# Performance work log

Measured on AMD Instinct MI355X. Metric: run time of the kernel, lower is better.

The kernel has to match this reference:

```python
import jax, jax.numpy as jnp
import numpy as np

EPS = 1e-7  # keras backend.epsilon()


def _conv_relu(x, w, b):
    # ConvNormRelu with BatchNorm folded into conv bias at inference
    y = jax.lax.conv_general_dilated(x, w, (1, 1), 'SAME',
                                     dimension_numbers=('NHWC', 'HWIO', 'NHWC'))
    return jax.nn.relu(y + b)


def _mlp(x, mw0, mb0, mw1, mb1, mw2, mb2):
    h = jax.nn.relu(x @ mw0 + mb0)
    h = jax.nn.relu(h @ mw1 + mb1)
    return h @ mw2 + mb2


def setup_inputs() -> dict:
    key = jax.random.key(0)
    ks = jax.random.split(key, 20)
    B, HQ = 2, 384
    feats2 = jax.random.normal(ks[0], (B, 192, 192, 64), jnp.float32)
    feats4 = jax.random.normal(ks[1], (B, 96, 96, 96), jnp.float32)
    feats32 = jax.random.normal(ks[2], (B, 24, 24, 160), jnp.float32)
    coords = jax.random.uniform(ks[3], (B, HQ, HQ, 2), jnp.float32, -1.0, 1.0)
    cells = jnp.full((B, HQ, HQ, 2), 2.0 / HQ, jnp.float32)
    s = 0.05
    params = dict(
        w2=jax.random.normal(ks[4], (1, 1, 64, 32)) * s, b2=jnp.zeros((32,)),
        w4=jax.random.normal(ks[5], (1, 1, 96, 32)) * s, b4=jnp.zeros((32,)),
        w32=jax.random.normal(ks[6], (1, 1, 160, 32)) * s, b32=jnp.zeros((32,)),
        wf=jax.random.normal(ks[7], (3, 3, 96, 96)) * s, bf=jnp.zeros((96,)),
        mw0=jax.random.normal(ks[8], (102, 64)) * s, mb0=jnp.zeros((64,)),
        mw1=jax.random.normal(ks[9], (64, 64)) * s, mb1=jnp.zeros((64,)),
        mw2=jax.random.normal(ks[10], (64, 1)) * s, mb2=jnp.zeros((1,)),
    )
    return dict(feats2=feats2, feats4=feats4, feats32=feats32,
                coords=coords, cells=cells, **params)


def reference(feats2, feats4, feats32, coords, cells,
              w2, b2, w4, b4, w32, b32, wf, bf,
              mw0, mb0, mw1, mb1, mw2, mb2):
    a2 = _conv_relu(feats2, w2, b2)
    a4 = _conv_relu(feats4, w4, b4)
    a32 = _conv_relu(feats32, w32, b32)
    B, H, W, _ = a2.shape
    # resize_by_sample: bilinear upsample to feats2 grid (half-pixel centers)
    a4 = jax.image.resize(a4, (B, H, W, a4.shape[-1]), method='bilinear')
    a32 = jax.image.resize(a32, (B, H, W, a32.shape[-1]), method='bilinear')
    aspp = _conv_relu(jnp.concatenate([a2, a4, a32], axis=-1), wf, bf)

    size = jnp.array([H, W], jnp.float32)
    rxry = 1.0 / size
    rel_cells = cells * size
    bi = jnp.arange(B)[:, None, None]  # batch gather index

    preds, areas = [], []
    for vy in (-1.0, 1.0):  # itertools.product([-1,1],[-1,1]) order
        for vx in (-1.0, 1.0):
            vv = jnp.array([vy, vx], jnp.float32)
            c = jnp.clip(coords + vv * rxry + EPS, -1.0 + EPS, 1.0 - EPS)
            # original reverses (y,x)->(x,y) for GridSample; index directly instead
            # nearest, align_corners=False: i = round((c+1)*N/2 - 0.5)
            iy = jnp.clip(jnp.round((c[..., 0] + 1.0) * H / 2.0 - 0.5).astype(jnp.int32), 0, H - 1)
            ix = jnp.clip(jnp.round((c[..., 1] + 1.0) * W / 2.0 - 0.5).astype(jnp.int32), 0, W - 1)
            feat_samp = aspp[bi, iy, ix]  # [B,HQ,WQ,96] irregular gather
            # nearest-sampling make_coord == analytic pixel centers of (iy,ix)
            coord_samp = jnp.stack(
                [((iy.astype(jnp.float32) + 0.5) / H) * 2.0 - 1.0,
                 ((ix.astype(jnp.float32) + 0.5) / W) * 2.0 - 1.0], axis=-1)
            rel = (coords - coord_samp) * size
            pred = _mlp(jnp.concatenate([feat_samp, rel, coords, rel_cells], axis=-1),
                        mw0, mb0, mw1, mb1, mw2, mb2)
            preds.append(pred)
            area = jnp.abs(jnp.prod(rel, axis=-1, keepdims=True)) + EPS
            areas.insert(0, area)  # pair each pred with opposite corner's area

    num = preds[0] * areas[0] + preds[1] * areas[1] + preds[2] * areas[2] + preds[3] * areas[3]
    den = areas[0] + areas[1] + areas[2] + areas[3]
    return num / den
```

## Files before the change

### kernel.cpp

```cpp
#include <hip/hip_runtime.h>
#include <math.h>


#define HQ 384
#define HA 192
#define NQ (2 * HQ * HQ)
#define NBS (NQ / 1024)
#define NBKT 288
#define NFLAT (NBKT * NBS)

typedef _Float16 half8  __attribute__((ext_vector_type(8)));
typedef _Float16 half4v __attribute__((ext_vector_type(4)));
typedef float    float4v __attribute__((ext_vector_type(4)));
typedef float    float16v __attribute__((ext_vector_type(16)));

__device__ __forceinline__ int bucket_id(int q, float cy, float cx) {
    const float LO = -1.0f + 1e-7f, HI = 1.0f - 1e-7f;
    const float RXY = 1.0f / (float)HA;
    float c0 = fminf(fmaxf((cy - RXY) + 1e-7f, LO), HI);
    float c1 = fminf(fmaxf((cx - RXY) + 1e-7f, LO), HI);
    int iy = (int)rintf(((c0 + 1.f) * (float)HA) * 0.5f - 0.5f);
    int ix = (int)rintf(((c1 + 1.f) * (float)HA) * 0.5f - 0.5f);
    iy = min(max(iy, 0), HA - 1);
    ix = min(max(ix, 0), HA - 1);
    int b = q / (HQ * HQ);
    return b * 144 + (iy >> 4) * 12 + (ix >> 4);
}

__launch_bounds__(1024)
__global__ void fused_front(const float* __restrict__ coords,
                            int* __restrict__ cntT,
                            unsigned short* __restrict__ lrank,
                            const float* __restrict__ mw0,
                            const float* __restrict__ mb0f,
                            const float* __restrict__ mw1,
                            const float* __restrict__ mb1f,
                            const float* __restrict__ wf,
                            _Float16* __restrict__ fragTab,
                            _Float16* __restrict__ fragTabW,
                            const float* __restrict__ feats4,
                            const float* __restrict__ w4,
                            const float* __restrict__ b4,
                            const float* __restrict__ feats32,
                            const float* __restrict__ w32,
                            const float* __restrict__ b32,
                            float* __restrict__ a4s,
                            float* __restrict__ a32s,
                            const float* __restrict__ feats2,
                            const float* __restrict__ w2,
                            const float* __restrict__ b2,
                            _Float16* __restrict__ xcatH) {
    const int blk = blockIdx.x;
    const int tid = threadIdx.x;

    if (blk < 288) {
        __shared__ int lh[NBKT];
        if (tid < NBKT) lh[tid] = 0;
        __syncthreads();
        const int q = blk * 1024 + tid;
        float cy = coords[(size_t)q * 2 + 0];
        float cx = coords[(size_t)q * 2 + 1];
        int r = atomicAdd(&lh[bucket_id(q, cy, cx)], 1);
        lrank[q] = (unsigned short)r;
        __syncthreads();
        if (tid < NBKT) cntT[tid * NBS + blk] = lh[tid];
    } else if (blk < 300) {
        int t = (blk - 288) * 1024 + tid;
        if (t < 1536) {
            int f = t >> 6, L = t & 63;
            int h = L >> 5;
            _Float16 vals[8];
            if (f < 14) {
                int ks = f >> 1, nt = f & 1;
                int col = nt * 32 + (L & 31);
#pragma unroll
                for (int j = 0; j < 8; ++j) {
                    int kk = ks * 16 + h * 8 + j;
                    float v = (kk < 102) ? mw0[kk * 64 + col]
                            : ((kk == 102) ? mb0f[col] : 0.f);
                    vals[j] = (_Float16)v;
                }
            } else {
                int g = f - 14;
                int ks = g >> 1, nt = g & 1;
                int col = nt * 32 + (L & 31);
#pragma unroll
                for (int j = 0; j < 8; ++j) {
                    int kp = ks * 16 + h * 8 + j;
                    float v;
                    if (ks < 4) {
                        int n = (kp & 0x33) | ((kp & 8) >> 1) | ((kp & 4) << 1);
                        v = mw1[n * 64 + col];
                    } else {
                        v = (kp == 64) ? mb1f[col] : 0.f;
                    }
                    vals[j] = (_Float16)v;
                }
            }
#pragma unroll
            for (int j = 0; j < 8; ++j) fragTab[t * 8 + j] = vals[j];
        } else {
            int tw = t - 1536;
            if (tw < 27 * 6 * 64) {
                int s   = tw / 384;
                int rem = tw - s * 384;
                int nt  = rem >> 6;
                int L   = rem & 63;
                int n_  = L & 15, qd = L >> 4;
                int tap = s / 3, kc = s - tap * 3;
#pragma unroll
                for (int j = 0; j < 8; ++j) {
                    int kch = kc * 32 + qd * 8 + j;
                    fragTabW[tw * 8 + j] =
                        (_Float16)wf[(tap * 96 + kch) * 96 + nt * 16 + n_];
                }
            }
        }
    } else if (blk < 444) {
        int t = (blk - 300) * 1024 + tid;
        int p = t >> 3, cg = t & 7;
        const float4v* xr = (const float4v*)(feats4 + (size_t)p * 96);
        float4v acc = *(const float4v*)(b4 + cg * 4);
#pragma unroll
        for (int i4 = 0; i4 < 24; ++i4) {
            float4v xv = xr[i4];
            const float* wr = w4 + (i4 * 4) * 32 + cg * 4;
#pragma unroll
            for (int j = 0; j < 4; ++j) {
                float4v wv = *(const float4v*)(wr + j * 32);
                acc[0] = fmaf(xv[j], wv[0], acc[0]);
                acc[1] = fmaf(xv[j], wv[1], acc[1]);
                acc[2] = fmaf(xv[j], wv[2], acc[2]);
                acc[3] = fmaf(xv[j], wv[3], acc[3]);
            }
        }
        float4v o = {fmaxf(acc[0], 0.f), fmaxf(acc[1], 0.f),
                     fmaxf(acc[2], 0.f), fmaxf(acc[3], 0.f)};
        *(float4v*)(a4s + (size_t)p * 32 + cg * 4) = o;
    } else if (blk < 453) {
        int t = (blk - 444) * 1024 + tid;
        if (t >= 1152 * 8) return;
        int p = t >> 3, cg = t & 7;
        const float4v* xr = (const float4v*)(feats32 + (size_t)p * 160);
        float4v acc = *(const float4v*)(b32 + cg * 4);
#pragma unroll
        for (int i4 = 0; i4 < 40; ++i4) {
            float4v xv = xr[i4];
            const float* wr = w32 + (i4 * 4) * 32 + cg * 4;
#pragma unroll
            for (int j = 0; j < 4; ++j) {
                float4v wv = *(const float4v*)(wr + j * 32);
                acc[0] = fmaf(xv[j], wv[0], acc[0]);
                acc[1] = fmaf(xv[j], wv[1], acc[1]);
                acc[2] = fmaf(xv[j], wv[2], acc[2]);
                acc[3] = fmaf(xv[j], wv[3], acc[3]);
            }
        }
        float4v o = {fmaxf(acc[0], 0.f), fmaxf(acc[1], 0.f),
                     fmaxf(acc[2], 0.f), fmaxf(acc[3], 0.f)};
        *(float4v*)(a32s + (size_t)p * 32 + cg * 4) = o;
    } else {
        int t = (blk - 453) * 1024 + tid;
        int p = t >> 3, cg = t & 7;
        const float4v* xr = (const float4v*)(feats2 + (size_t)p * 64);
        float4v acc = *(const float4v*)(b2 + cg * 4);
#pragma unroll
        for (int i4 = 0; i4 < 16; ++i4) {
            float4v xv = xr[i4];
            const float* wr = w2 + (i4 * 4) * 32 + cg * 4;
#pragma unroll
            for (int j = 0; j < 4; ++j) {
                float4v wv = *(const float4v*)(wr + j * 32);
                acc[0] = fmaf(xv[j], wv[0], acc[0]);
                acc[1] = fmaf(xv[j], wv[1], acc[1]);
                acc[2] = fmaf(xv[j], wv[2], acc[2]);
                acc[3] = fmaf(xv[j], wv[3], acc[3]);
            }
        }
        half4v h;
        h[0] = (_Float16)fmaxf(acc[0], 0.f);
        h[1] = (_Float16)fmaxf(acc[1], 0.f);
        h[2] = (_Float16)fmaxf(acc[2], 0.f);
        h[3] = (_Float16)fmaxf(acc[3], 0.f);
        *(half4v*)(xcatH + (size_t)p * 96 + cg * 4) = h;
    }
}

__launch_bounds__(1024)
__global__ void fused_mid(const int* __restrict__ cntT,
                          int* __restrict__ scanEx,
                          int* __restrict__ chunkTot,
                          const float* __restrict__ a4s,
                          const float* __restrict__ a32s,
                          _Float16* __restrict__ xcatH) {
    const int blk = blockIdx.x;
    const int t = threadIdx.x;

    if (blk < 81) {
        __shared__ int s[1024];
        const int gi = blk * 1024 + t;
        int v = cntT[gi];
        s[t] = v;
        __syncthreads();
        for (int off = 1; off < 1024; off <<= 1) {
            int x = (t >= off) ? s[t - off] : 0;
            __syncthreads();
            s[t] += x;
            __syncthreads();
        }
        scanEx[gi] = s[t] - v;
        if (t == 1023) chunkTot[blk] = s[t];
        return;
    }

    const int z = (blk < 81 + 576) ? 1 : 2;
    int tt = ((z == 1) ? (blk - 81) : (blk - 657)) * 1024 + t;
    int p = tt >> 3, cg = tt & 7;

    const float* src = (z == 1) ? a4s : a32s;
    const int   S    = (z == 1) ? 96 : 24;
    const float inv  = (z == 1) ? 0.5f : 0.125f;
    const int   coff = (z == 1) ? 32 : 64;

    int x = p % HA;
    int r = p / HA;
    int y = r % HA;
    int b = r / HA;

    float u = ((float)y + 0.5f) * inv - 0.5f;
    float v = ((float)x + 0.5f) * inv - 0.5f;
    float fu = floorf(u), fv = floorf(v);
    float wu = u - fu, wv = v - fv;
    int y0 = (int)fu, x0 = (int)fv;
    int y1 = min(y0 + 1, S - 1);
    int x1 = min(x0 + 1, S - 1);
    y0 = max(y0, 0);
    x0 = max(x0, 0);

    const float* sb = src + (size_t)b * S * S * 32 + cg * 4;
    float4v v00 = *(const float4v*)(sb + (y0 * S + x0) * 32);
    float4v v01 = *(const float4v*)(sb + (y0 * S + x1) * 32);
    float4v v10 = *(const float4v*)(sb + (y1 * S + x0) * 32);
    float4v v11 = *(const float4v*)(sb + (y1 * S + x1) * 32);
    half4v h;
#pragma unroll
    for (int j = 0; j < 4; ++j) {
        float t0 = v00[j] * (1.f - wu) + v10[j] * wu;
        float t1 = v01[j] * (1.f - wu) + v11[j] * wu;
        h[j] = (_Float16)(t0 * (1.f - wv) + t1 * wv);
    }
    *(half4v*)(xcatH + (size_t)p * 96 + coff + cg * 4) = h;
}

__launch_bounds__(256, 4)
__global__ void fused_back(const _Float16* __restrict__ xH,
                           const _Float16* __restrict__ fragTabW,
                           const float* __restrict__ bias,
                           _Float16* __restrict__ yH,
                           const float* __restrict__ coords,
                           const float* __restrict__ cells,
                           const int* __restrict__ scanEx,
                           const int* __restrict__ chunkTot,
                           const unsigned short* __restrict__ lrank,
                           int* __restrict__ qidx,
                           float4v* __restrict__ qdata) {
    __shared__ __align__(16) unsigned char smemU[37440];
    const int blk = blockIdx.x;
    const int tid = threadIdx.x;

    if (blk < 576) {
        _Float16* lds = (_Float16*)smemU;
        const int lane = tid & 63;
        const int wv   = tid >> 6;
        const int n_   = lane & 15;
        const int qd   = lane >> 4;
        const int nh   = wv & 1;
        const int yg   = wv >> 1;
        const int bx0  = (blk % 12) * 16;
        const int by0  = ((blk / 12) % 24) * 8;
        const int b    = blk / 288;

        for (int idx = tid; idx < 2160; idx += 256) {
            int hy  = idx / 216;
            int rem = idx - hy * 216;
            int hx  = rem / 12;
            int cc  = rem - hx * 12;
            int gy = by0 + hy - 1, gx = bx0 + hx - 1;
            half8 v = {(_Float16)0.f, (_Float16)0.f, (_Float16)0.f, (_Float16)0.f,
                       (_Float16)0.f, (_Float16)0.f, (_Float16)0.f, (_Float16)0.f};
            if (gy >= 0 && gy < HA && gx >= 0 && gx < HA)
                v = *(const half8*)(xH + (((size_t)b * HA + gy) * HA + gx) * 96 + cc * 8);
            *(half8*)&lds[(hy * 18 + hx) * 104 + cc * 8] = v;
        }

        float bv[3];
#pragma unroll
        for (int j = 0; j < 3; ++j) bv[j] = bias[(nh * 3 + j) * 16 + n_];

        __syncthreads();

        float4v acc[4][3];
#pragma unroll
        for (int r = 0; r < 4; ++r)
#pragma unroll
            for (int j = 0; j < 3; ++j) {
                float4v z = {0.f, 0.f, 0.f, 0.f};
                acc[r][j] = z;
            }

#pragma unroll 1
        for (int ky = 0; ky < 3; ++ky)
#pragma unroll 1
            for (int kx = 0; kx < 3; ++kx) {
                const int tap = ky * 3 + kx;
#pragma unroll
                for (int kc = 0; kc < 3; ++kc) {
                    const int s = tap * 3 + kc;
                    half8 bf[3];
#pragma unroll
                    for (int j = 0; j < 3; ++j)
                        bf[j] = *(const half8*)(fragTabW +
                                ((size_t)(s * 6 + nh * 3 + j) * 64 + lane) * 8);
#pragma unroll
                    for (int r = 0; r < 4; ++r) {
                        const int yr = yg * 4 + r;
                        half8 a = *(const half8*)&lds[((yr + ky) * 18 + (n_ + kx)) * 104
                                                      + kc * 32 + qd * 8];
#pragma unroll
                        for (int j = 0; j < 3; ++j)
                            acc[r][j] = __builtin_amdgcn_mfma_f32_16x16x32_f16(
                                a, bf[j], acc[r][j], 0, 0, 0);
                    }
                }
            }

#pragma unroll
        for (int r = 0; r < 4; ++r) {
            const int gy = by0 + yg * 4 + r;
#pragma unroll
            for (int j = 0; j < 3; ++j) {
                const int ch = (nh * 3 + j) * 16 + n_;
#pragma unroll
                for (int reg = 0; reg < 4; ++reg) {
                    const int gx = bx0 + qd * 4 + reg;
                    yH[(((size_t)b * HA + gy) * HA + gx) * 96 + ch] =
                        (_Float16)fmaxf(acc[r][j][reg] + bv[j], 0.f);
                }
            }
        }
    } else {
        int* pEx = (int*)smemU;
        int v = 0;
        if (tid < 81) v = chunkTot[tid];
        if (tid < 128) pEx[tid] = v;
        __syncthreads();
        for (int off = 1; off < 128; off <<= 1) {
            int x = 0;
            if (tid < 128 && tid >= off) x = pEx[tid - off];
            __syncthreads();
            if (tid < 128) pEx[tid] += x;
            __syncthreads();
        }
        if (tid < 128) pEx[tid] -= v;
        __syncthreads();

        const int q = (blk - 576) * 256 + tid;
        float cy = coords[(size_t)q * 2 + 0];
        float cx = coords[(size_t)q * 2 + 1];
        int bkt = bucket_id(q, cy, cx);
        int sb  = q >> 10;
        int li  = bkt * NBS + sb;
        int pos = pEx[li >> 10] + scanEx[li] + (int)lrank[q];
        qidx[pos] = q;
        float4v d = {cy, cx,
                     cells[(size_t)q * 2 + 0] * (float)HA,
                     cells[(size_t)q * 2 + 1] * (float)HA};
        qdata[pos] = d;
    }
}

__launch_bounds__(1024, 8)
__global__ void decoder_mlp_mfma(const _Float16* __restrict__ asppH,
                                 const int* __restrict__ qidx,
                                 const float4v* __restrict__ qdata,
                                 const _Float16* __restrict__ fragTab,
                                 const float* __restrict__ mw2,
                                 const float* __restrict__ mb2,
                                 float* __restrict__ out) {
    __shared__ __align__(16) _Float16 fragL[24 * 64 * 8];
    __shared__ __align__(16) float biasL[68];

    const int tid  = threadIdx.x;
    const int lane = tid & 63;
    const int wv   = tid >> 6;
    const int h    = lane >> 5;
    const int col  = lane & 31;
    const int R    = (blockIdx.x & 7) * 288 + (blockIdx.x >> 3);

    const int sp = R * 128 + wv * 8 + (col >> 2);
    const float4v d = qdata[sp];
    const int   qq = qidx[sp];
    const int   b  = qq / (HQ * HQ);
    const float cy = d[0], cx = d[1], rcy = d[2], rcx = d[3];
    const int   k  = col & 3;

    const float LO = -1.0f + 1e-7f, HI = 1.0f - 1e-7f;
    const float RXY = 1.0f / (float)HA;
    const float vy = (k < 2) ? -1.f : 1.f;
    const float vx = (k & 1) ? 1.f : -1.f;

    float c0 = fminf(fmaxf((cy + vy * RXY) + 1e-7f, LO), HI);
    float c1 = fminf(fmaxf((cx + vx * RXY) + 1e-7f, LO), HI);
    int iy = (int)rintf(((c0 + 1.f) * (float)HA) * 0.5f - 0.5f);
    int ix = (int)rintf(((c1 + 1.f) * (float)HA) * 0.5f - 0.5f);
    iy = min(max(iy, 0), HA - 1);
    ix = min(max(ix, 0), HA - 1);

    const float cs0 = (((float)iy + 0.5f) / (float)HA) * 2.f - 1.f;
    const float cs1 = (((float)ix + 0.5f) / (float)HA) * 2.f - 1.f;
    const float r0 = (cy - cs0) * (float)HA;
    const float r1 = (cx - cs1) * (float)HA;
    const float area = fabsf(r0 * r1) + 1e-7f;
    const int   pix = ((b * HA + iy) * HA + ix) * 96;

    half8 Xf[3];
    Xf[0] = *(const half8*)(asppH + pix + 0 * 16 + h * 8);
    Xf[1] = *(const half8*)(asppH + pix + 1 * 16 + h * 8);
    Xf[2] = *(const half8*)(asppH + pix + 2 * 16 + h * 8);

#pragma unroll
    for (int it = 0; it < 2; ++it) {
        const int i = it * 1024 + tid;
        if (i < 1536)
            *(half8*)&fragL[i * 8] = *(const half8*)(fragTab + (size_t)i * 8);
    }
    if (tid < 64) biasL[tid] = mw2[tid];
    if (tid == 0) biasL[64] = mb2[0];
    __syncthreads();

    float16v acc[2];
    {
        float16v z{};
        acc[0] = z;
        acc[1] = z;
    }
#pragma unroll
    for (int ks = 0; ks < 3; ++ks)
#pragma unroll
        for (int nt = 0; nt < 2; ++nt) {
            half8 w0 = *(const half8*)&fragL[((ks * 2 + nt) * 64 + lane) * 8];
            acc[nt] = __builtin_amdgcn_mfma_f32_32x32x16_f16(w0, Xf[ks],
                                                             acc[nt], 0, 0, 0);
        }

    Xf[0] = *(const half8*)(asppH + pix + 3 * 16 + h * 8);
    Xf[1] = *(const half8*)(asppH + pix + 4 * 16 + h * 8);
    Xf[2] = *(const half8*)(asppH + pix + 5 * 16 + h * 8);
#pragma unroll
    for (int ks = 0; ks < 3; ++ks)
#pragma unroll
        for (int nt = 0; nt < 2; ++nt) {
            half8 w0 = *(const half8*)&fragL[(((ks + 3) * 2 + nt) * 64 + lane) * 8];
            acc[nt] = __builtin_amdgcn_mfma_f32_32x32x16_f16(w0, Xf[ks],
                                                             acc[nt], 0, 0, 0);
        }
    {
        half8 e = {(_Float16)0.f, (_Float16)0.f, (_Float16)0.f, (_Float16)0.f,
                   (_Float16)0.f, (_Float16)0.f, (_Float16)0.f, (_Float16)0.f};
        if (h == 0) {
            e[0] = (_Float16)r0;  e[1] = (_Float16)r1;
            e[2] = (_Float16)cy;  e[3] = (_Float16)cx;
            e[4] = (_Float16)rcy; e[5] = (_Float16)rcx;
            e[6] = (_Float16)1.f;
        }
#pragma unroll
        for (int nt = 0; nt < 2; ++nt) {
            half8 w0 = *(const half8*)&fragL[((6 * 2 + nt) * 64 + lane) * 8];
            acc[nt] = __builtin_amdgcn_mfma_f32_32x32x16_f16(w0, e,
                                                             acc[nt], 0, 0, 0);
        }
    }

    half8 b1f[5];
#pragma unroll
    for (int ks = 0; ks < 4; ++ks) {
        half8 t;
#pragma unroll
        for (int j = 0; j < 8; ++j)
            t[j] = (_Float16)fmaxf(acc[ks >> 1][(ks & 1) * 8 + j], 0.f);
        b1f[ks] = t;
    }
    {
        half8 e = {(_Float16)0.f, (_Float16)0.f, (_Float16)0.f, (_Float16)0.f,
                   (_Float16)0.f, (_Float16)0.f, (_Float16)0.f, (_Float16)0.f};
        if (h == 0) e[0] = (_Float16)1.f;
        b1f[4] = e;
    }

    float16v acc1[2];
    {
        float16v z{};
        acc1[0] = z;
        acc1[1] = z;
    }
#pragma unroll
    for (int ks = 0; ks < 5; ++ks)
#pragma unroll
        for (int nt = 0; nt < 2; ++nt) {
            half8 w1 = *(const half8*)&fragL[(((14 + ks * 2 + nt)) * 64 + lane) * 8];
            acc1[nt] = __builtin_amdgcn_mfma_f32_32x32x16_f16(w1, b1f[ks],
                                                              acc1[nt], 0, 0, 0);
        }

    float s = 0.f;
#pragma unroll
    for (int nt = 0; nt < 2; ++nt)
#pragma unroll
        for (int q = 0; q < 4; ++q) {
            float4v w2v = *(const float4v*)&biasL[nt * 32 + q * 8 + h * 4];
#pragma unroll
            for (int i = 0; i < 4; ++i)
                s = fmaf(fmaxf(acc1[nt][q * 4 + i], 0.f), w2v[i], s);
        }
    s += __shfl_xor(s, 32, 64);
    const float p = s + biasL[64];

    float a_opp = __shfl_xor(area, 3, 64);
    float np = p * a_opp;
    float dp = area;
    np += __shfl_xor(np, 1, 64);
    dp += __shfl_xor(dp, 1, 64);
    np += __shfl_xor(np, 2, 64);
    dp += __shfl_xor(dp, 2, 64);

    if ((lane & 0x23) == 0)
        out[qq] = np / dp;
}

extern "C" void kernel_launch(void* const* d_in, const int* in_sizes, int n_in,
                              void* d_out, int out_size, void* d_ws, size_t ws_size,
                              hipStream_t stream) {
    (void)in_sizes; (void)n_in; (void)out_size; (void)ws_size;
    const float* feats2  = (const float*)d_in[0];
    const float* feats4  = (const float*)d_in[1];
    const float* feats32 = (const float*)d_in[2];
    const float* coords  = (const float*)d_in[3];
    const float* cells   = (const float*)d_in[4];
    const float* w2  = (const float*)d_in[5];
    const float* b2  = (const float*)d_in[6];
    const float* w4  = (const float*)d_in[7];
    const float* b4  = (const float*)d_in[8];
    const float* w32 = (const float*)d_in[9];
    const float* b32 = (const float*)d_in[10];
    const float* wf  = (const float*)d_in[11];
    const float* bf  = (const float*)d_in[12];
    const float* mw0 = (const float*)d_in[13];
    const float* mb0 = (const float*)d_in[14];
    const float* mw1 = (const float*)d_in[15];
    const float* mb1 = (const float*)d_in[16];
    const float* mw2 = (const float*)d_in[17];
    const float* mb2 = (const float*)d_in[18];

    float* ws = (float*)d_ws;
    float*    a4s   = ws;
    float*    a32s  = a4s + 589824;
    _Float16* xcatH = (_Float16*)(a32s + 36864);
    _Float16* asppH = xcatH + 7077888;
    _Float16* fragTab  = asppH + 7077888;
    _Float16* fragTabW = fragTab + 12288;
    float4v*  qdata = (float4v*)(fragTabW + 82944);
    int*      qidx  = (int*)(qdata + NQ);
    int*      cntT  = qidx + NQ;
    int*      scanEx = cntT + NFLAT;
    int*      chunkTot = scanEx + NFLAT;
    unsigned short* lrank = (unsigned short*)(chunkTot + 128);
    float* out = (float*)d_out;

    fused_front<<<1029, 1024, 0, stream>>>(coords, cntT, lrank,
                                           mw0, mb0, mw1, mb1, wf,
                                           fragTab, fragTabW,
                                           feats4, w4, b4, feats32, w32, b32,
                                           a4s, a32s, feats2, w2, b2, xcatH);
    fused_mid<<<1233, 1024, 0, stream>>>(cntT, scanEx, chunkTot,
                                         a4s, a32s, xcatH);
    fused_back<<<1728, 256, 0, stream>>>(xcatH, fragTabW, bf, asppH,
                                         coords, cells, scanEx, chunkTot,
                                         lrank, qidx, qdata);
    decoder_mlp_mfma<<<2304, 1024, 0, stream>>>(asppH, qidx, qdata, fragTab,
                                                mw2, mb2, out);
}
```

Before: 193.1 us.

## Fuse bilinear upsampling of a4/a32 into the 3x3 conv halo load

```diff
diff --git a/kernel.cpp b/kernel.cpp
--- a/kernel.cpp
+++ b/kernel.cpp
@@ -189,71 +189,29 @@
 __launch_bounds__(1024)
 __global__ void fused_mid(const int* __restrict__ cntT,
                           int* __restrict__ scanEx,
-                          int* __restrict__ chunkTot,
-                          const float* __restrict__ a4s,
-                          const float* __restrict__ a32s,
-                          _Float16* __restrict__ xcatH) {
+                          int* __restrict__ chunkTot) {
     const int blk = blockIdx.x;
     const int t = threadIdx.x;
 
-    if (blk < 81) {
-        __shared__ int s[1024];
-        const int gi = blk * 1024 + t;
-        int v = cntT[gi];
-        s[t] = v;
-        __syncthreads();
-        for (int off = 1; off < 1024; off <<= 1) {
-            int x = (t >= off) ? s[t - off] : 0;
-            __syncthreads();
-            s[t] += x;
-            __syncthreads();
-        }
-        scanEx[gi] = s[t] - v;
-        if (t == 1023) chunkTot[blk] = s[t];
-        return;
-    }
-
-    const int z = (blk < 81 + 576) ? 1 : 2;
-    int tt = ((z == 1) ? (blk - 81) : (blk - 657)) * 1024 + t;
-    int p = tt >> 3, cg = tt & 7;
-
-    const float* src = (z == 1) ? a4s : a32s;
-    const int   S    = (z == 1) ? 96 : 24;
-    const float inv  = (z == 1) ? 0.5f : 0.125f;
-    const int   coff = (z == 1) ? 32 : 64;
-
-    int x = p % HA;
-    int r = p / HA;
-    int y = r % HA;
-    int b = r / HA;
-
-    float u = ((float)y + 0.5f) * inv - 0.5f;
-    float v = ((float)x + 0.5f) * inv - 0.5f;
-    float fu = floorf(u), fv = floorf(v);
-    float wu = u - fu, wv = v - fv;
-    int y0 = (int)fu, x0 = (int)fv;
-    int y1 = min(y0 + 1, S - 1);
-    int x1 = min(x0 + 1, S - 1);
-    y0 = max(y0, 0);
-    x0 = max(x0, 0);
-
-    const float* sb = src + (size_t)b * S * S * 32 + cg * 4;
-    float4v v00 = *(const float4v*)(sb + (y0 * S + x0) * 32);
-    float4v v01 = *(const float4v*)(sb + (y0 * S + x1) * 32);
-    float4v v10 = *(const float4v*)(sb + (y1 * S + x0) * 32);
-    float4v v11 = *(const float4v*)(sb + (y1 * S + x1) * 32);
-    half4v h;
-#pragma unroll
-    for (int j = 0; j < 4; ++j) {
-        float t0 = v00[j] * (1.f - wu) + v10[j] * wu;
-        float t1 = v01[j] * (1.f - wu) + v11[j] * wu;
-        h[j] = (_Float16)(t0 * (1.f - wv) + t1 * wv);
-    }
-    *(half4v*)(xcatH + (size_t)p * 96 + coff + cg * 4) = h;
+    __shared__ int s[1024];
+    const int gi = blk * 1024 + t;
+    int v = cntT[gi];
+    s[t] = v;
+    __syncthreads();
+    for (int off = 1; off < 1024; off <<= 1) {
+        int x = (t >= off) ? s[t - off] : 0;
+        __syncthreads();
+        s[t] += x;
+        __syncthreads();
+    }
+    scanEx[gi] = s[t] - v;
+    if (t == 1023) chunkTot[blk] = s[t];
 }
 
 __launch_bounds__(256, 4)
 __global__ void fused_back(const _Float16* __restrict__ xH,
+                           const float* __restrict__ a4s,
+                           const float* __restrict__ a32s,
                            const _Float16* __restrict__ fragTabW,
                            const float* __restrict__ bias,
                            _Float16* __restrict__ yH,
@@ -288,8 +246,42 @@
             int gy = by0 + hy - 1, gx = bx0 + hx - 1;
             half8 v = {(_Float16)0.f, (_Float16)0.f, (_Float16)0.f, (_Float16)0.f,
                        (_Float16)0.f, (_Float16)0.f, (_Float16)0.f, (_Float16)0.f};
-            if (gy >= 0 && gy < HA && gx >= 0 && gx < HA)
-                v = *(const half8*)(xH + (((size_t)b * HA + gy) * HA + gx) * 96 + cc * 8);
+            if (gy >= 0 && gy < HA && gx >= 0 && gx < HA) {
+                if (cc < 4) {
+                    v = *(const half8*)(xH + (((size_t)b * HA + gy) * HA + gx) * 96 + cc * 8);
+                } else {
+                    const int  z2  = (cc >= 8);
+                    const float* src = z2 ? a32s : a4s;
+                    const int  S   = z2 ? 24 : 96;
+                    const float inv = z2 ? 0.125f : 0.5f;
+                    const int  c0  = (z2 ? (cc - 8) : (cc - 4)) * 8;
+
+                    float u = ((float)gy + 0.5f) * inv - 0.5f;
+                    float w = ((float)gx + 0.5f) * inv - 0.5f;
+                    float fu = floorf(u), fv = floorf(w);
+                    float wu = u - fu, wv2 = w - fv;
+                    int y0 = (int)fu, x0 = (int)fv;
+                    int y1 = min(y0 + 1, S - 1);
+                    int x1 = min(x0 + 1, S - 1);
+                    y0 = max(y0, 0);
+                    x0 = max(x0, 0);
+                    const float* sb = src + (size_t)b * S * S * 32;
+#pragma unroll
+                    for (int g2 = 0; g2 < 2; ++g2) {
+                        const float* sc = sb + c0 + g2 * 4;
+                        float4v v00 = *(const float4v*)(sc + (y0 * S + x0) * 32);
+                        float4v v01 = *(const float4v*)(sc + (y0 * S + x1) * 32);
+                        float4v v10 = *(const float4v*)(sc + (y1 * S + x0) * 32);
+                        float4v v11 = *(const float4v*)(sc + (y1 * S + x1) * 32);
+#pragma unroll
+                        for (int j = 0; j < 4; ++j) {
+                            float t0 = v00[j] * (1.f - wu) + v10[j] * wu;
+                            float t1 = v01[j] * (1.f - wu) + v11[j] * wu;
+                            v[g2 * 4 + j] = (_Float16)(t0 * (1.f - wv2) + t1 * wv2);
+                        }
+                    }
+                }
+            }
             *(half8*)&lds[(hy * 18 + hx) * 104 + cc * 8] = v;
         }
 
@@ -581,9 +573,8 @@
                                            fragTab, fragTabW,
                                            feats4, w4, b4, feats32, w32, b32,
                                            a4s, a32s, feats2, w2, b2, xcatH);
-    fused_mid<<<1233, 1024, 0, stream>>>(cntT, scanEx, chunkTot,
-                                         a4s, a32s, xcatH);
-    fused_back<<<1728, 256, 0, stream>>>(xcatH, fragTabW, bf, asppH,
+    fused_mid<<<81, 1024, 0, stream>>>(cntT, scanEx, chunkTot);
+    fused_back<<<1728, 256, 0, stream>>>(xcatH, a4s, a32s, fragTabW, bf, asppH,
                                          coords, cells, scanEx, chunkTot,
                                          lrank, qidx, qdata);
     decoder_mlp_mfma<<<2304, 1024, 0, stream>>>(asppH, qidx, qdata, fragTab,
```

Measured after the change: 196.1 us. No clear change (+1.5%).
